# Kernel tuning notes

Measured on AMD Instinct MI355X. Metric: run time of the kernel, lower is better.

## Reference

```python
import jax, jax.numpy as jnp
import numpy as np

B, N_LINKS, N_JOINTS, C_L, C_J = 4096, 33, 32, 64, 128

def setup_inputs() -> dict:
    key = jax.random.key(0)
    k1, k2, k3, k4 = jax.random.split(key, 4)
    link_feats = jax.random.normal(k1, (B, N_LINKS, C_L, 16), dtype=jnp.float32)
    joint_feats = jax.random.normal(k2, (B, N_JOINTS, C_J), dtype=jnp.float32)
    # Stacked per-joint Linear weights: [J, C_L*16, C_J], bias [J, C_J]
    fan_in = C_L * 16
    W = jax.random.normal(k3, (N_JOINTS, fan_in, C_J), dtype=jnp.float32) / np.sqrt(fan_in).astype(np.float32)
    b = jax.random.normal(k4, (N_JOINTS, C_J), dtype=jnp.float32) * 0.01
    child_idx = jnp.arange(1, N_JOINTS + 1, dtype=jnp.int64)  # child link of joint j is link j+1
    return {"link_feats": link_feats, "joint_feats": joint_feats, "W": W, "b": b, "child_idx": child_idx}

def reference(link_feats, joint_feats, W, b, child_idx):
    # Gather child-link features per joint: [B, J, C_L, 16] -> flatten to [B, J, C_L*16]
    Bsz = link_feats.shape[0]
    J = child_idx.shape[0]
    x = link_feats[:, child_idx].reshape(Bsz, J, -1)
    # Grouped GEMM over joints (replaces Python loop of tiny Linears), + bias + residual
    return jnp.einsum('bji,jio->bjo', x, W) + b[None, :, :] + joint_feats
```

## Files before the change

### kernel.cpp

```cpp
#include <hip/hip_runtime.h>

typedef __attribute__((ext_vector_type(8))) short bf16x8;
typedef __attribute__((ext_vector_type(4))) short bf16x4;
typedef __attribute__((ext_vector_type(4))) float f32x4;

#define NB    4096
#define NLINK 33
#define NJ    32
#define KTOT  1024
#define CJ    128
#define BM    32
#define BKF   256
#define NMAC  (KTOT / BKF)

__device__ short g_Wf[NJ * KTOT * CJ];

static __device__ __forceinline__ short f2bf(float f) {
    unsigned u = __builtin_bit_cast(unsigned, f);
    unsigned r = u + 0x7FFFu + ((u >> 16) & 1u);
    return (short)(r >> 16);
}

__global__ __launch_bounds__(256) void conv_w(const float* __restrict__ W) {
    const int gid = blockIdx.x * 256 + threadIdx.x;
    const int q  = gid & 3;
    const int c  = (gid >> 2) & 127;
    const int kt = (gid >> 9) & 31;
    const int j  = gid >> 14;
    const float* src = W + ((size_t)j * KTOT + kt * 32 + q * 8) * CJ + c;
    bf16x8 v;
    #pragma unroll
    for (int e = 0; e < 8; ++e) v[e] = f2bf(src[(size_t)e * CJ]);
    reinterpret_cast<bf16x8*>(g_Wf)[gid] = v;
}

__global__ __launch_bounds__(256, 3) void joint_gemm(
    const float* __restrict__ link,
    const float* __restrict__ jf,
    const float* __restrict__ bias,
    const int*   __restrict__ child,
    float* __restrict__ out)
{
    __shared__ short lA[BM * BKF];

    const int tid  = threadIdx.x;
    const int lane = tid & 63;
    const int wave = tid >> 6;
    const int q    = lane >> 4;
    const int r    = lane & 15;

    const int bx = blockIdx.x;
    const int j  = bx & 31;
    const int mt = bx >> 5;
    const int row0 = mt * BM;
    const int cidx = child[j];

    const int srow = tid >> 3;
    const int li   = tid & 7;
    const float* abase = link + ((size_t)(row0 + srow) * NLINK + cidx) * KTOT + 4 * li;
    short* lw0 = lA + (((li >> 1) * 32 + srow) * 8 + (li & 1) * 4);

    const bf16x8* wb = reinterpret_cast<const bf16x8*>(g_Wf);
    const size_t bb = ((size_t)j * 32 * 128 + wave * 32 + r) * 4 + q;

    f32x4  acc[2][2] = {};
    float4 Ar[8];

    auto loadA = [&](int m) {
        #pragma unroll
        for (int i = 0; i < 8; ++i)
            Ar[i] = *reinterpret_cast<const float4*>(abase + m * BKF + 32 * i);
    };

    loadA(0);

    for (int m = 0; m < NMAC; ++m) {
        __syncthreads();
        #pragma unroll
        for (int i = 0; i < 8; ++i) {
            bf16x4 v;
            v[0] = f2bf(Ar[i].x); v[1] = f2bf(Ar[i].y);
            v[2] = f2bf(Ar[i].z); v[3] = f2bf(Ar[i].w);
            *reinterpret_cast<bf16x4*>(lw0 + i * 1024) = v;
        }
        __syncthreads();

        bf16x8 Ball[16];
        #pragma unroll
        for (int ks = 0; ks < 8; ++ks) {
            Ball[2 * ks]     = wb[bb + (size_t)(m * 8 + ks) * 512];
            Ball[2 * ks + 1] = wb[bb + (size_t)(m * 8 + ks) * 512 + 64];
        }
        if (m + 1 < NMAC) loadA(m + 1);

        #pragma unroll
        for (int ks = 0; ks < 8; ++ks) {
            const short* cb = lA + ((ks * 4 + q) * 32 + r) * 8;
            bf16x8 a0 = *reinterpret_cast<const bf16x8*>(cb);
            bf16x8 a1 = *reinterpret_cast<const bf16x8*>(cb + 16 * 8);
            acc[0][0] = __builtin_amdgcn_mfma_f32_16x16x32_bf16(a0, Ball[2 * ks],     acc[0][0], 0, 0, 0);
            acc[0][1] = __builtin_amdgcn_mfma_f32_16x16x32_bf16(a0, Ball[2 * ks + 1], acc[0][1], 0, 0, 0);
            acc[1][0] = __builtin_amdgcn_mfma_f32_16x16x32_bf16(a1, Ball[2 * ks],     acc[1][0], 0, 0, 0);
            acc[1][1] = __builtin_amdgcn_mfma_f32_16x16x32_bf16(a1, Ball[2 * ks + 1], acc[1][1], 0, 0, 0);
        }
    }

    float bv[2];
    bv[0] = bias[j * CJ + wave * 32 + r];
    bv[1] = bias[j * CJ + wave * 32 + 16 + r];

    #pragma unroll
    for (int mi = 0; mi < 2; ++mi) {
        #pragma unroll
        for (int rr = 0; rr < 4; ++rr) {
            const int bg = row0 + mi * 16 + q * 4 + rr;
            const size_t ob = ((size_t)bg * NJ + j) * CJ + wave * 32;
            #pragma unroll
            for (int ni = 0; ni < 2; ++ni) {
                const int o = ni * 16 + r;
                out[ob + o] = acc[mi][ni][rr] + bv[ni] + jf[ob + o];
            }
        }
    }
}

extern "C" void kernel_launch(void* const* d_in, const int* in_sizes, int n_in,
                              void* d_out, int out_size, void* d_ws, size_t ws_size,
                              hipStream_t stream) {
    (void)in_sizes; (void)n_in; (void)out_size; (void)d_ws; (void)ws_size;
    const float* link  = (const float*)d_in[0];
    const float* jfeat = (const float*)d_in[1];
    const float* W     = (const float*)d_in[2];
    const float* bias  = (const float*)d_in[3];
    const int*   child = (const int*)d_in[4];
    float* out = (float*)d_out;

    conv_w<<<dim3((NJ * KTOT * CJ / 8) / 256), dim3(256), 0, stream>>>(W);
    joint_gemm<<<dim3(NJ * (NB / BM)), dim3(256), 0, stream>>>(link, jfeat, bias, child, out);
}
```

Baseline: 173.6 us.

## Stage full K tile of A in swizzled LDS and reshape wave tiling

Loads the whole 32x1024 A tile into LDS once, converting to bf16 with 16-byte stores and an XOR swizzle to avoid bank conflicts. It then runs a single fully unrolled 32-step MFMA loop with no per-chunk barriers. Waves are rearranged into a 2x2 grid of 16 rows by 64 columns, so each wave reads one A fragment and four B fragments per step. The jf residual and bias are prefetched before the loop. The cost is 64KB of LDS per block and lower occupancy (launch bounds drop from 3 to 2), and there is no longer any overlap between global A loads and compute.

After: 237.8 us. 36.9% more time.

```diff
diff --git a/kernel.cpp b/kernel.cpp
--- a/kernel.cpp
+++ b/kernel.cpp
@@ -1,7 +1,6 @@
 #include <hip/hip_runtime.h>
 
 typedef __attribute__((ext_vector_type(8))) short bf16x8;
-typedef __attribute__((ext_vector_type(4))) short bf16x4;
 typedef __attribute__((ext_vector_type(4))) float f32x4;
 
 #define NB    4096
@@ -10,8 +9,6 @@
 #define KTOT  1024
 #define CJ    128
 #define BM    32
-#define BKF   256
-#define NMAC  (KTOT / BKF)
 
 __device__ short g_Wf[NJ * KTOT * CJ];
 
@@ -34,93 +31,88 @@
     reinterpret_cast<bf16x8*>(g_Wf)[gid] = v;
 }
 
-__global__ __launch_bounds__(256, 3) void joint_gemm(
+__global__ __launch_bounds__(256, 2) void joint_gemm(
     const float* __restrict__ link,
     const float* __restrict__ jf,
     const float* __restrict__ bias,
     const int*   __restrict__ child,
     float* __restrict__ out)
 {
-    __shared__ short lA[BM * BKF];
+    __shared__ short lA[BM * 1024];
 
     const int tid  = threadIdx.x;
     const int lane = tid & 63;
     const int wave = tid >> 6;
+    const int wr   = wave >> 1;
+    const int wc   = wave & 1;
     const int q    = lane >> 4;
     const int r    = lane & 15;
 
-    const int bx = blockIdx.x;
-    const int j  = bx & 31;
-    const int mt = bx >> 5;
+    const int j  = blockIdx.x & 31;
+    const int mt = blockIdx.x >> 5;
     const int row0 = mt * BM;
     const int cidx = child[j];
 
-    const int srow = tid >> 3;
-    const int li   = tid & 7;
-    const float* abase = link + ((size_t)(row0 + srow) * NLINK + cidx) * KTOT + 4 * li;
-    short* lw0 = lA + (((li >> 1) * 32 + srow) * 8 + (li & 1) * 4);
+    {
+        const int srow = tid & 31;
+        const int sk   = tid >> 5;
+        const float* ab = link + ((size_t)(row0 + srow) * NLINK + cidx) * KTOT;
+        short* lrow = lA + srow * 1024;
+        const int skey = 4 * (srow & 15);
+        #pragma unroll
+        for (int i = 0; i < 16; ++i) {
+            const int cell = i * 8 + sk;
+            const float4 f0 = *reinterpret_cast<const float4*>(ab + cell * 8);
+            const float4 f1 = *reinterpret_cast<const float4*>(ab + cell * 8 + 4);
+            bf16x8 v;
+            v[0] = f2bf(f0.x); v[1] = f2bf(f0.y); v[2] = f2bf(f0.z); v[3] = f2bf(f0.w);
+            v[4] = f2bf(f1.x); v[5] = f2bf(f1.y); v[6] = f2bf(f1.z); v[7] = f2bf(f1.w);
+            *reinterpret_cast<bf16x8*>(lrow + (cell ^ skey) * 8) = v;
+        }
+    }
+    __syncthreads();
 
     const bf16x8* wb = reinterpret_cast<const bf16x8*>(g_Wf);
-    const size_t bb = ((size_t)j * 32 * 128 + wave * 32 + r) * 4 + q;
+    const size_t bb = (size_t)j * 16384 + ((size_t)wc * 64 + r) * 4 + q;
 
-    f32x4  acc[2][2] = {};
-    float4 Ar[8];
-
-    auto loadA = [&](int m) {
+    float bv[4];
+    float jv[4][4];
+    {
         #pragma unroll
-        for (int i = 0; i < 8; ++i)
-            Ar[i] = *reinterpret_cast<const float4*>(abase + m * BKF + 32 * i);
-    };
-
-    loadA(0);
-
-    for (int m = 0; m < NMAC; ++m) {
-        __syncthreads();
+        for (int nb = 0; nb < 4; ++nb) bv[nb] = bias[j * CJ + wc * 64 + nb * 16 + r];
         #pragma unroll
-        for (int i = 0; i < 8; ++i) {
-            bf16x4 v;
-            v[0] = f2bf(Ar[i].x); v[1] = f2bf(Ar[i].y);
-            v[2] = f2bf(Ar[i].z); v[3] = f2bf(Ar[i].w);
-            *reinterpret_cast<bf16x4*>(lw0 + i * 1024) = v;
-        }
-        __syncthreads();
-
-        bf16x8 Ball[16];
-        #pragma unroll
-        for (int ks = 0; ks < 8; ++ks) {
-            Ball[2 * ks]     = wb[bb + (size_t)(m * 8 + ks) * 512];
-            Ball[2 * ks + 1] = wb[bb + (size_t)(m * 8 + ks) * 512 + 64];
-        }
-        if (m + 1 < NMAC) loadA(m + 1);
-
-        #pragma unroll
-        for (int ks = 0; ks < 8; ++ks) {
-            const short* cb = lA + ((ks * 4 + q) * 32 + r) * 8;
-            bf16x8 a0 = *reinterpret_cast<const bf16x8*>(cb);
-            bf16x8 a1 = *reinterpret_cast<const bf16x8*>(cb + 16 * 8);
-            acc[0][0] = __builtin_amdgcn_mfma_f32_16x16x32_bf16(a0, Ball[2 * ks],     acc[0][0], 0, 0, 0);
-            acc[0][1] = __builtin_amdgcn_mfma_f32_16x16x32_bf16(a0, Ball[2 * ks + 1], acc[0][1], 0, 0, 0);
-            acc[1][0] = __builtin_amdgcn_mfma_f32_16x16x32_bf16(a1, Ball[2 * ks],     acc[1][0], 0, 0, 0);
-            acc[1][1] = __builtin_amdgcn_mfma_f32_16x16x32_bf16(a1, Ball[2 * ks + 1], acc[1][1], 0, 0, 0);
+        for (int rr = 0; rr < 4; ++rr) {
+            const int bg = row0 + wr * 16 + q * 4 + rr;
+            const size_t ob = ((size_t)bg * NJ + j) * CJ + wc * 64;
+            #pragma unroll
+            for (int nb = 0; nb < 4; ++nb) jv[rr][nb] = jf[ob + nb * 16 + r];
         }
     }
 
-    float bv[2];
-    bv[0] = bias[j * CJ + wave * 32 + r];
-    bv[1] = bias[j * CJ + wave * 32 + 16 + r];
+    f32x4 acc[4] = {};
+    const short* arow = lA + (wr * 16 + r) * 1024;
+    const int rkey = 4 * r;
 
     #pragma unroll
-    for (int mi = 0; mi < 2; ++mi) {
+    for (int ks = 0; ks < 32; ++ks) {
+        const bf16x8 af = *reinterpret_cast<const bf16x8*>(arow + ((ks * 4 + q) ^ rkey) * 8);
+        const bf16x8 b0 = wb[bb + (size_t)ks * 512];
+        const bf16x8 b1 = wb[bb + (size_t)ks * 512 + 64];
+        const bf16x8 b2 = wb[bb + (size_t)ks * 512 + 128];
+        const bf16x8 b3 = wb[bb + (size_t)ks * 512 + 192];
+        acc[0] = __builtin_amdgcn_mfma_f32_16x16x32_bf16(af, b0, acc[0], 0, 0, 0);
+        acc[1] = __builtin_amdgcn_mfma_f32_16x16x32_bf16(af, b1, acc[1], 0, 0, 0);
+        acc[2] = __builtin_amdgcn_mfma_f32_16x16x32_bf16(af, b2, acc[2], 0, 0, 0);
+        acc[3] = __builtin_amdgcn_mfma_f32_16x16x32_bf16(af, b3, acc[3], 0, 0, 0);
+    }
+
+    #pragma unroll
+    for (int rr = 0; rr < 4; ++rr) {
+        const int bg = row0 + wr * 16 + q * 4 + rr;
+        const size_t ob = ((size_t)bg * NJ + j) * CJ + wc * 64;
         #pragma unroll
-        for (int rr = 0; rr < 4; ++rr) {
-            const int bg = row0 + mi * 16 + q * 4 + rr;
-            const size_t ob = ((size_t)bg * NJ + j) * CJ + wave * 32;
-            #pragma unroll
-            for (int ni = 0; ni < 2; ++ni) {
-                const int o = ni * 16 + r;
-                out[ob + o] = acc[mi][ni][rr] + bv[ni] + jf[ob + o];
-            }
-        }
+        for (int nb = 0; nb < 4; ++nb)
+            out[ob + nb * 16 + r] = acc[nb][rr] + bv[nb] + jv[rr][nb];
     }
 }
 
```
